# Performance work log

Hardware: AMD Instinct MI355X
Metric: run time of the kernel (lower is better)

The kernel has to match this reference:

```python
import jax, jax.numpy as jnp
import numpy as np

EPS = 1e-5
N_NODES = 100000
C_IN = 128
C_OUT = 128
N_EDGES = 3200000


def setup_inputs() -> dict:
    key = jax.random.key(0)
    k1, k2, k3 = jax.random.split(key, 3)
    x = jax.random.normal(k1, (N_NODES, C_IN), dtype=jnp.float32)
    edge_index = jax.random.randint(k2, (2, N_EDGES), 0, N_NODES, dtype=jnp.int64)
    # BatchNorm1d affine params
    gamma = jnp.ones((C_IN,), dtype=jnp.float32)
    beta = jnp.zeros((C_IN,), dtype=jnp.float32)
    # GCNConv linear weight (glorot) and bias
    limit = np.sqrt(6.0 / (C_IN + C_OUT)).astype(np.float32)
    W = jax.random.uniform(k3, (C_IN, C_OUT), minval=-limit, maxval=limit, dtype=jnp.float32)
    b = jnp.zeros((C_OUT,), dtype=jnp.float32)
    return {"x": x, "edge_index": edge_index, "gamma": gamma, "beta": beta, "W": W, "b": b}


def reference(x, edge_index, gamma, beta, W, b):
    n = x.shape[0]
    # --- BatchNorm1d (training mode: batch statistics, biased variance) ---
    mean = jnp.mean(x, axis=0)
    var = jnp.mean(jnp.square(x - mean), axis=0)
    xn = (x - mean) * jax.lax.rsqrt(var + EPS) * gamma + beta
    # --- GCNConv: linear, add self-loops, symmetric normalization, scatter-add ---
    h = xn @ W  # [n, C_out]
    loops = jnp.arange(n, dtype=edge_index.dtype)
    row = jnp.concatenate([edge_index[0], loops])  # source nodes
    col = jnp.concatenate([edge_index[1], loops])  # target nodes
    deg = jax.ops.segment_sum(jnp.ones_like(col, dtype=h.dtype), col, num_segments=n)
    dis = jnp.where(deg > 0, jax.lax.rsqrt(jnp.maximum(deg, 1.0)), 0.0)
    norm = dis[row] * dis[col]  # [E+n]
    msg = h[row] * norm[:, None]  # gather + scale
    out = jax.ops.segment_sum(msg, col, num_segments=n) + b  # scatter-add
    return jax.nn.relu(out)
```

## Files before the change

kernel.cpp:

```cpp
#include <hip/hip_runtime.h>

#define EPS_BN 1e-5f
#define C 128
#define CG 32
#define CAP 6144
#define NBLK 256

__device__ inline unsigned bf16_rne(float f) {
  unsigned u = __float_as_uint(f);
  return (u + 0x7FFFu + ((u >> 16) & 1u)) >> 16;
}

__global__ void k_init(float* __restrict__ sums) {
  int i = blockIdx.x * blockDim.x + threadIdx.x;
  if (i < 256) sums[i] = 0.0f;
}

__global__ void k_stats(const float4* __restrict__ x4, float* __restrict__ sums, int n) {
  __shared__ float4 s_s[256];
  __shared__ float4 s_q[256];
  int t = threadIdx.x;
  int cg = t & 31;
  int rl = t >> 5;
  float4 s = make_float4(0.f, 0.f, 0.f, 0.f);
  float4 q = make_float4(0.f, 0.f, 0.f, 0.f);
  for (int r = blockIdx.x * 8 + rl; r < n; r += gridDim.x * 8) {
    float4 v = x4[(size_t)r * CG + cg];
    s.x += v.x; s.y += v.y; s.z += v.z; s.w += v.w;
    q.x += v.x * v.x; q.y += v.y * v.y; q.z += v.z * v.z; q.w += v.w * v.w;
  }
  s_s[t] = s; s_q[t] = q;
  __syncthreads();
  if (t < 32) {
    for (int j = 1; j < 8; ++j) {
      float4 a = s_s[t + 32 * j];
      float4 b = s_q[t + 32 * j];
      s.x += a.x; s.y += a.y; s.z += a.z; s.w += a.w;
      q.x += b.x; q.y += b.y; q.z += b.z; q.w += b.w;
    }
    atomicAdd(&sums[t * 4 + 0], s.x);
    atomicAdd(&sums[t * 4 + 1], s.y);
    atomicAdd(&sums[t * 4 + 2], s.z);
    atomicAdd(&sums[t * 4 + 3], s.w);
    atomicAdd(&sums[C + t * 4 + 0], q.x);
    atomicAdd(&sums[C + t * 4 + 1], q.y);
    atomicAdd(&sums[C + t * 4 + 2], q.z);
    atomicAdd(&sums[C + t * 4 + 3], q.w);
  }
}

__global__ void k_finalize(const float* __restrict__ sums,
                           const float* __restrict__ gamma,
                           const float* __restrict__ beta,
                           float* __restrict__ scale, float* __restrict__ shift,
                           int n) {
  int c = threadIdx.x;
  if (c < C) {
    float inv_n = 1.0f / (float)n;
    float mean = sums[c] * inv_n;
    float var = sums[C + c] * inv_n - mean * mean;
    float rstd = rsqrtf(var + EPS_BN);
    float sc = gamma[c] * rstd;
    scale[c] = sc;
    shift[c] = beta[c] - mean * sc;
  }
}

__global__ void k_hist(const int* __restrict__ col, int* __restrict__ histG,
                       int E, int NB, int chunk) {
  __shared__ int h[800];
  int b = blockIdx.x, t = threadIdx.x;
  for (int i = t; i < NB; i += 256) h[i] = 0;
  __syncthreads();
  int s = b * chunk, eend = min(E, s + chunk);
  for (int e = s + t; e < eend; e += 256) atomicAdd(&h[col[e] >> 7], 1);
  __syncthreads();
  for (int i = t; i < NB; i += 256) histG[b * NB + i] = h[i];
}

__global__ void k_scanH(int* __restrict__ histG, int* __restrict__ btot, int NB) {
  __shared__ int sh[NBLK];
  int q = blockIdx.x, t = threadIdx.x;
  int v = histG[t * NB + q];
  sh[t] = v;
  __syncthreads();
  for (int off = 1; off < NBLK; off <<= 1) {
    int a = (t >= off) ? sh[t - off] : 0;
    __syncthreads();
    sh[t] += a;
    __syncthreads();
  }
  histG[t * NB + q] = sh[t] - v;
  if (t == NBLK - 1) btot[q] = sh[t];
}

__global__ void k_scanB(const int* __restrict__ btot, int* __restrict__ boffs,
                        int NB, int E) {
  __shared__ int sh[1024];
  int t = threadIdx.x;
  int v = (t < NB) ? btot[t] : 0;
  sh[t] = v;
  __syncthreads();
  for (int off = 1; off < 1024; off <<= 1) {
    int a = (t >= off) ? sh[t - off] : 0;
    __syncthreads();
    sh[t] += a;
    __syncthreads();
  }
  if (t < NB) boffs[t] = sh[t] - v;
  if (t == 0) boffs[NB] = E;
}

__global__ void k_part(const int* __restrict__ row, const int* __restrict__ col,
                       const int* __restrict__ histG, const int* __restrict__ boffs,
                       unsigned* __restrict__ binned, int E, int NB, int chunk) {
  __shared__ int cur[800];
  int b = blockIdx.x, t = threadIdx.x;
  for (int i = t; i < NB; i += 256) cur[i] = boffs[i] + histG[b * NB + i];
  __syncthreads();
  int s = b * chunk, eend = min(E, s + chunk);
  for (int e = s + t; e < eend; e += 256) {
    int c = col[e];
    int pos = atomicAdd(&cur[c >> 7], 1);
    binned[pos] = ((unsigned)(c & 127) << 17) | (unsigned)row[e];
  }
}

__global__ __launch_bounds__(256) void k_reorder(
    unsigned* __restrict__ binned, const int* __restrict__ boffs,
    int* __restrict__ noffs, float* __restrict__ dis, int n, int E) {
  __shared__ int cnt[128];
  __shared__ int offs[128];
  __shared__ int cur[128];
  __shared__ int scn[128];
  __shared__ unsigned list[CAP];
  int b = blockIdx.x, t = threadIdx.x;
  if (t < 128) cnt[t] = 0;
  __syncthreads();
  int s = boffs[b], e = boffs[b + 1];
  for (int i = s + t; i < e; i += 256) atomicAdd(&cnt[binned[i] >> 17], 1);
  __syncthreads();
  if (t < 128) scn[t] = cnt[t];
  __syncthreads();
  for (int off = 1; off < 128; off <<= 1) {
    int a = (t >= off && t < 128) ? scn[t - off] : 0;
    __syncthreads();
    if (t < 128) scn[t] += a;
    __syncthreads();
  }
  if (t < 128) {
    offs[t] = scn[t] - cnt[t];
    cur[t] = scn[t] - cnt[t];
  }
  __syncthreads();
  for (int i = s + t; i < e; i += 256) {
    unsigned v = binned[i];
    int pos = atomicAdd(&cur[v >> 17], 1);
    if (pos < CAP) list[pos] = v & 0x1FFFFu;
  }
  __syncthreads();
  int len = e - s;
  for (int i = t; i < len; i += 256) binned[s + i] = list[i];
  int node = b * 128 + t;
  if (t < 128 && node < n) {
    noffs[node] = s + offs[t];
    dis[node] = rsqrtf((float)(cnt[t] + 1));
  }
  if (b == 0 && t == 0) noffs[n] = E;
}

__global__ void k_prep(const float2* __restrict__ x2, const float* __restrict__ dis,
                       const float2* __restrict__ scale2,
                       const float2* __restrict__ shift2,
                       unsigned* __restrict__ y, int n) {
  int idx = blockIdx.x * blockDim.x + threadIdx.x;
  int r = idx >> 6;
  if (r >= n) return;
  int lane = idx & 63;
  float d = dis[r];
  float2 v = x2[(size_t)r * 64 + lane];
  float2 sc = scale2[lane], sh = shift2[lane];
  float y0 = (v.x * sc.x + sh.x) * d;
  float y1 = (v.y * sc.y + sh.y) * d;
  y[(size_t)r * 64 + lane] = (bf16_rne(y1) << 16) | bf16_rne(y0);
}

__global__ __launch_bounds__(256) void k_G(
    const unsigned* __restrict__ y, const unsigned* __restrict__ lst,
    const int* __restrict__ noffs, const float* __restrict__ dis,
    const float2* __restrict__ x2, const float2* __restrict__ scale2,
    const float2* __restrict__ shift2, float2* __restrict__ out2,
    int n, int useY) {
  int w = (blockIdx.x * blockDim.x + threadIdx.x) >> 6;
  if (w >= n) return;
  int lane = threadIdx.x & 63;
  int s = noffs[w], t = noffs[w + 1];
  float2 a0 = make_float2(0.f, 0.f), a1 = make_float2(0.f, 0.f);
  float2 a2 = make_float2(0.f, 0.f), a3 = make_float2(0.f, 0.f);
  if (useY) {
    int i = s;
    for (; i + 3 < t; i += 4) {
      int r0 = lst[i], r1 = lst[i + 1], r2 = lst[i + 2], r3 = lst[i + 3];
      unsigned u0 = y[(size_t)r0 * 64 + lane];
      unsigned u1 = y[(size_t)r1 * 64 + lane];
      unsigned u2 = y[(size_t)r2 * 64 + lane];
      unsigned u3 = y[(size_t)r3 * 64 + lane];
      a0.x += __uint_as_float(u0 << 16); a0.y += __uint_as_float(u0 & 0xFFFF0000u);
      a1.x += __uint_as_float(u1 << 16); a1.y += __uint_as_float(u1 & 0xFFFF0000u);
      a2.x += __uint_as_float(u2 << 16); a2.y += __uint_as_float(u2 & 0xFFFF0000u);
      a3.x += __uint_as_float(u3 << 16); a3.y += __uint_as_float(u3 & 0xFFFF0000u);
    }
    for (; i < t; ++i) {
      unsigned u = y[(size_t)lst[i] * 64 + lane];
      a0.x += __uint_as_float(u << 16); a0.y += __uint_as_float(u & 0xFFFF0000u);
    }
    float dc = dis[w];
    float2 o;
    o.x = dc * (a0.x + a1.x + a2.x + a3.x);
    o.y = dc * (a0.y + a1.y + a2.y + a3.y);
    out2[(size_t)w * 64 + lane] = o;
  } else {
    float sd = 0.f;
    for (int i = s; i < t; ++i) {
      int r = lst[i];
      float d = dis[r];
      float2 v = x2[(size_t)r * 64 + lane];
      a0.x += v.x * d; a0.y += v.y * d; sd += d;
    }
    float dc = dis[w];
    float2 sc = scale2[lane], sh = shift2[lane];
    float2 o;
    o.x = dc * (a0.x * sc.x + sd * sh.x);
    o.y = dc * (a0.y * sc.y + sd * sh.y);
    out2[(size_t)w * 64 + lane] = o;
  }
}

__global__ __launch_bounds__(256) void k_gemm(float* __restrict__ out,
                        const float4* __restrict__ x4,
                        const float* __restrict__ W,
                        const float* __restrict__ bias,
                        const float* __restrict__ scale,
                        const float* __restrict__ shift,
                        const float* __restrict__ dis, int n) {
  __shared__ float sW[64 * C];
  __shared__ float sG[32 * C];
  int t = threadIdx.x;
  int rowBase = blockIdx.x * 32;

  const float4* scale4 = (const float4*)scale;
  const float4* shift4 = (const float4*)shift;
  float4* sG4 = (float4*)sG;
  float4* sW4 = (float4*)sW;
  const float4* W4 = (const float4*)W;
  const float4* out4 = (const float4*)out;

  for (int i = t; i < 32 * CG; i += 256) {
    int r = i >> 5, g = i & 31;
    int rw = rowBase + r;
    float4 acc = make_float4(0.f, 0.f, 0.f, 0.f);
    if (rw < n) {
      acc = out4[(size_t)rw * CG + g];
      float4 xv = x4[(size_t)rw * CG + g];
      float d = dis[rw];
      float inv = d * d;
      float4 sc = scale4[g];
      float4 sh = shift4[g];
      acc.x += (xv.x * sc.x + sh.x) * inv;
      acc.y += (xv.y * sc.y + sh.y) * inv;
      acc.z += (xv.z * sc.z + sh.z) * inv;
      acc.w += (xv.w * sc.w + sh.w) * inv;
    }
    sG4[i] = acc;
  }

  int tx = t & 127;
  int ty = t >> 7;
  float acc[16];
#pragma unroll
  for (int i = 0; i < 16; ++i) acc[i] = 0.f;

  for (int kc = 0; kc < 2; ++kc) {
    for (int i = t; i < 64 * C / 4; i += 256) sW4[i] = W4[kc * 2048 + i];
    __syncthreads();
#pragma unroll 4
    for (int k = 0; k < 64; ++k) {
      float w = sW[k * C + tx];
#pragma unroll
      for (int rr = 0; rr < 16; ++rr)
        acc[rr] += sG[(rr * 2 + ty) * C + kc * 64 + k] * w;
    }
    __syncthreads();
  }

  float bv = bias[tx];
#pragma unroll
  for (int rr = 0; rr < 16; ++rr) {
    int rw = rowBase + rr * 2 + ty;
    if (rw < n) {
      float o = acc[rr] + bv;
      out[(size_t)rw * C + tx] = o > 0.f ? o : 0.f;
    }
  }
}

extern "C" void kernel_launch(void* const* d_in, const int* in_sizes, int n_in,
                              void* d_out, int out_size, void* d_ws, size_t ws_size,
                              hipStream_t stream) {
  const float* x = (const float*)d_in[0];
  const int* edge = (const int*)d_in[1];
  const float* gamma = (const float*)d_in[2];
  const float* beta = (const float*)d_in[3];
  const float* W = (const float*)d_in[4];
  const float* bias = (const float*)d_in[5];
  float* out = (float*)d_out;

  int n = in_sizes[0] / C;
  int E = in_sizes[1] / 2;
  int NB = (n + 127) / 128;
  int chunk = (E + NBLK - 1) / NBLK;

  float* ws = (float*)d_ws;
  float* sums = ws;
  float* scale = ws + 256;
  float* shift = ws + 384;
  float* dis = ws + 512;
  int* btot = (int*)(ws + 512 + n);
  int* boffs = btot + NB;
  int* noffs = boffs + NB + 1;
  int* histG = noffs + n + 1;
  unsigned* binned = (unsigned*)(histG + (size_t)NBLK * NB);
  unsigned* y = binned + E;

  size_t need = (size_t)512 + n + NB + (NB + 1) + (n + 1) +
                (size_t)NBLK * NB + E + (size_t)n * 64;
  int useY = (ws_size >= need * 4) ? 1 : 0;

  k_init<<<1, 256, 0, stream>>>(sums);
  k_stats<<<256, 256, 0, stream>>>((const float4*)x, sums, n);
  k_finalize<<<1, 128, 0, stream>>>(sums, gamma, beta, scale, shift, n);
  k_hist<<<NBLK, 256, 0, stream>>>(edge + E, histG, E, NB, chunk);
  k_scanH<<<NB, NBLK, 0, stream>>>(histG, btot, NB);
  k_scanB<<<1, 1024, 0, stream>>>(btot, boffs, NB, E);
  k_part<<<NBLK, 256, 0, stream>>>(edge, edge + E, histG, boffs, binned, E, NB, chunk);
  k_reorder<<<NB, 256, 0, stream>>>(binned, boffs, noffs, dis, n, E);
  if (useY) {
    k_prep<<<(n * 64 + 255) / 256, 256, 0, stream>>>(
        (const float2*)x, dis, (const float2*)scale, (const float2*)shift, y, n);
  }
  k_G<<<(n * 64 + 255) / 256, 256, 0, stream>>>(
      y, binned, noffs, dis, (const float2*)x, (const float2*)scale,
      (const float2*)shift, (float2*)out, n, useY);
  k_gemm<<<(n + 31) / 32, 256, 0, stream>>>(out, (const float4*)x, W, bias,
                                            scale, shift, dis, n);
}
```

Before: 376.9 us.

## Replace final GEMM with bf16 MFMA using hi/lo split aggregated features

The aggregation kernel now writes its normalized sums as a pair of bf16 arrays (high part plus residual) instead of fp32 into the output buffer. A new GEMM kernel loads these and a bf16 copy of W into shared memory and runs 16x16x32 bf16 MFMA instructions twice per tile to recover near-fp32 accuracy, fusing bias and ReLU. The intent is to move the dense 128x128 transform from the presumably scalar/FP32 path onto matrix cores and to cut the fp32 intermediate traffic. It needs extra workspace, falls back to the old path if that is not available, and rounds W to bf16, which loses some accuracy.

```diff
diff --git a/kernel.cpp b/kernel.cpp
--- a/kernel.cpp
+++ b/kernel.cpp
@@ -6,10 +6,14 @@
 #define CAP 6144
 #define NBLK 256
 
+typedef __attribute__((ext_vector_type(8))) short bf16x8;
+typedef __attribute__((ext_vector_type(4))) float f32x4;
+
 __device__ inline unsigned bf16_rne(float f) {
   unsigned u = __float_as_uint(f);
   return (u + 0x7FFFu + ((u >> 16) & 1u)) >> 16;
 }
+__device__ inline float bf16_f(unsigned h) { return __uint_as_float(h << 16); }
 
 __global__ void k_init(float* __restrict__ sums) {
   int i = blockIdx.x * blockDim.x + threadIdx.x;
@@ -183,6 +187,102 @@
   float y0 = (v.x * sc.x + sh.x) * d;
   float y1 = (v.y * sc.y + sh.y) * d;
   y[(size_t)r * 64 + lane] = (bf16_rne(y1) << 16) | bf16_rne(y0);
+}
+
+__global__ __launch_bounds__(256) void k_G2(
+    const unsigned* __restrict__ y, const unsigned* __restrict__ lst,
+    const int* __restrict__ noffs, const float* __restrict__ dis,
+    unsigned* __restrict__ ghi, unsigned* __restrict__ glo, int n) {
+  int w = (blockIdx.x * blockDim.x + threadIdx.x) >> 6;
+  if (w >= n) return;
+  int lane = threadIdx.x & 63;
+  int s = noffs[w], t = noffs[w + 1];
+  float2 a0 = make_float2(0.f, 0.f), a1 = make_float2(0.f, 0.f);
+  float2 a2 = make_float2(0.f, 0.f), a3 = make_float2(0.f, 0.f);
+  int i = s;
+  for (; i + 3 < t; i += 4) {
+    int r0 = lst[i], r1 = lst[i + 1], r2 = lst[i + 2], r3 = lst[i + 3];
+    unsigned u0 = y[(size_t)r0 * 64 + lane];
+    unsigned u1 = y[(size_t)r1 * 64 + lane];
+    unsigned u2 = y[(size_t)r2 * 64 + lane];
+    unsigned u3 = y[(size_t)r3 * 64 + lane];
+    a0.x += __uint_as_float(u0 << 16); a0.y += __uint_as_float(u0 & 0xFFFF0000u);
+    a1.x += __uint_as_float(u1 << 16); a1.y += __uint_as_float(u1 & 0xFFFF0000u);
+    a2.x += __uint_as_float(u2 << 16); a2.y += __uint_as_float(u2 & 0xFFFF0000u);
+    a3.x += __uint_as_float(u3 << 16); a3.y += __uint_as_float(u3 & 0xFFFF0000u);
+  }
+  for (; i < t; ++i) {
+    unsigned u = y[(size_t)lst[i] * 64 + lane];
+    a0.x += __uint_as_float(u << 16); a0.y += __uint_as_float(u & 0xFFFF0000u);
+  }
+  unsigned uw = y[(size_t)w * 64 + lane];
+  a0.x += __uint_as_float(uw << 16); a0.y += __uint_as_float(uw & 0xFFFF0000u);
+  float dc = dis[w];
+  float gx = dc * (a0.x + a1.x + a2.x + a3.x);
+  float gy = dc * (a0.y + a1.y + a2.y + a3.y);
+  unsigned hx = bf16_rne(gx), hy = bf16_rne(gy);
+  unsigned lx = bf16_rne(gx - bf16_f(hx)), ly = bf16_rne(gy - bf16_f(hy));
+  size_t o = (size_t)w * 64 + lane;
+  ghi[o] = (hy << 16) | hx;
+  glo[o] = (ly << 16) | lx;
+}
+
+__global__ __launch_bounds__(256) void k_gemmM(
+    const unsigned* __restrict__ ghi, const unsigned* __restrict__ glo,
+    const float* __restrict__ W, const float* __restrict__ bias,
+    float* __restrict__ out, int n) {
+  __shared__ __align__(16) unsigned short sGh[64][136];
+  __shared__ __align__(16) unsigned short sGl[64][136];
+  __shared__ __align__(16) unsigned short sWt[128][136];
+  int t = threadIdx.x;
+  int rowBase = blockIdx.x * 64;
+  for (int i = t; i < 16384; i += 256) {
+    int k = i >> 7, c = i & 127;
+    sWt[c][k] = (unsigned short)bf16_rne(W[i]);
+  }
+  for (int i = t; i < 4096; i += 256) {
+    int r = i >> 6, c = i & 63;
+    int rw = rowBase + r;
+    unsigned uh = 0, ul = 0;
+    if (rw < n) {
+      uh = ghi[(size_t)rw * 64 + c];
+      ul = glo[(size_t)rw * 64 + c];
+    }
+    *(unsigned*)&sGh[r][c * 2] = uh;
+    *(unsigned*)&sGl[r][c * 2] = ul;
+  }
+  __syncthreads();
+  int w = t >> 6, l = t & 63;
+  int m16 = l & 15, kb = l >> 4;
+  int rtile = w * 16;
+  f32x4 acc[8];
+#pragma unroll
+  for (int i = 0; i < 8; ++i) acc[i] = (f32x4){0.f, 0.f, 0.f, 0.f};
+#pragma unroll
+  for (int kt = 0; kt < 4; ++kt) {
+    int koff = kt * 32 + kb * 8;
+    bf16x8 ah = *(const bf16x8*)&sGh[rtile + m16][koff];
+    bf16x8 al = *(const bf16x8*)&sGl[rtile + m16][koff];
+#pragma unroll
+    for (int nt = 0; nt < 8; ++nt) {
+      bf16x8 bb = *(const bf16x8*)&sWt[nt * 16 + m16][koff];
+      acc[nt] = __builtin_amdgcn_mfma_f32_16x16x32_bf16(ah, bb, acc[nt], 0, 0, 0);
+      acc[nt] = __builtin_amdgcn_mfma_f32_16x16x32_bf16(al, bb, acc[nt], 0, 0, 0);
+    }
+  }
+#pragma unroll
+  for (int nt = 0; nt < 8; ++nt) {
+    int colc = nt * 16 + m16;
+    float bv = bias[colc];
+#pragma unroll
+    for (int reg = 0; reg < 4; ++reg) {
+      int row = rowBase + rtile + kb * 4 + reg;
+      if (row < n) {
+        float o = acc[nt][reg] + bv;
+        out[(size_t)row * C + colc] = fmaxf(o, 0.f);
+      }
+    }
+  }
 }
 
 __global__ __launch_bounds__(256) void k_G(
@@ -331,10 +431,14 @@
   int* histG = noffs + n + 1;
   unsigned* binned = (unsigned*)(histG + (size_t)NBLK * NB);
   unsigned* y = binned + E;
-
-  size_t need = (size_t)512 + n + NB + (NB + 1) + (n + 1) +
-                (size_t)NBLK * NB + E + (size_t)n * 64;
-  int useY = (ws_size >= need * 4) ? 1 : 0;
+  unsigned* ghi = y + (size_t)n * 64;
+  unsigned* glo = ghi + (size_t)n * 64;
+
+  size_t base = (size_t)512 + n + NB + (NB + 1) + (n + 1) +
+                (size_t)NBLK * NB + E;
+  size_t need_old = base + (size_t)n * 64;
+  size_t need_new = base + (size_t)n * 64 * 3;
+  int mode = (ws_size >= need_new * 4) ? 2 : (ws_size >= need_old * 4) ? 1 : 0;
 
   k_init<<<1, 256, 0, stream>>>(sums);
   k_stats<<<256, 256, 0, stream>>>((const float4*)x, sums, n);
@@ -344,13 +448,19 @@
   k_scanB<<<1, 1024, 0, stream>>>(btot, boffs, NB, E);
   k_part<<<NBLK, 256, 0, stream>>>(edge, edge + E, histG, boffs, binned, E, NB, chunk);
   k_reorder<<<NB, 256, 0, stream>>>(binned, boffs, noffs, dis, n, E);
-  if (useY) {
+  if (mode >= 1) {
     k_prep<<<(n * 64 + 255) / 256, 256, 0, stream>>>(
         (const float2*)x, dis, (const float2*)scale, (const float2*)shift, y, n);
   }
-  k_G<<<(n * 64 + 255) / 256, 256, 0, stream>>>(
-      y, binned, noffs, dis, (const float2*)x, (const float2*)scale,
-      (const float2*)shift, (float2*)out, n, useY);
-  k_gemm<<<(n + 31) / 32, 256, 0, stream>>>(out, (const float4*)x, W, bias,
-                                            scale, shift, dis, n);
-}
+  if (mode == 2) {
+    k_G2<<<(n * 64 + 255) / 256, 256, 0, stream>>>(y, binned, noffs, dis,
+                                                   ghi, glo, n);
+    k_gemmM<<<(n + 63) / 64, 256, 0, stream>>>(ghi, glo, W, bias, out, n);
+  } else {
+    k_G<<<(n * 64 + 255) / 256, 256, 0, stream>>>(
+        y, binned, noffs, dis, (const float2*)x, (const float2*)scale,
+        (const float2*)shift, (float2*)out, n, mode);
+    k_gemm<<<(n + 31) / 32, 256, 0, stream>>>(out, (const float4*)x, W, bias,
+                                              scale, shift, dis, n);
+  }
+}
```

Measured after the change: 349.0 us. 7.4% less time.
